# Kernel tuning notes

Hardware: AMD Instinct MI355X
Metric: run time of the kernel (lower is better)

Reference implementation:

```python
import jax, jax.numpy as jnp
import numpy as np

TOP_K = 8
H, E, I = 2048, 64, 768  # hidden, experts, moe_intermediate


def setup_inputs() -> dict:
    key = jax.random.key(0)
    k1, k2, k3, k4 = jax.random.split(key, 4)
    hidden_states = jax.random.normal(k1, (2, 256, H), dtype=jnp.float32)
    gate_w = jax.random.normal(k2, (E, H), dtype=jnp.float32) * 0.02   # nn.Linear(H, E).weight
    w13 = jax.random.normal(k3, (E, 2 * I, H), dtype=jnp.float32) * 0.02  # [E, 2I, H]
    w2 = jax.random.normal(k4, (E, H, I), dtype=jnp.float32) * 0.02       # [E, H, I]
    return {"hidden_states": hidden_states, "gate_w": gate_w, "w13": w13, "w2": w2}


def reference(hidden_states, gate_w, w13, w2):
    orig_shape = hidden_states.shape
    x = hidden_states.reshape(-1, orig_shape[-1])  # [M, H]
    M = x.shape[0]
    num_experts = gate_w.shape[0]

    # Router: logits -> fp32 softmax -> top-k -> renormalize
    router_logits = x @ gate_w.T  # [M, E]
    routing_weights = jax.nn.softmax(router_logits.astype(jnp.float32), axis=-1)
    topk_w, topk_ids = jax.lax.top_k(routing_weights, TOP_K)  # [M, K]
    topk_w = topk_w / jnp.sum(topk_w, axis=-1, keepdims=True)

    # Scatter top-k weights into a dense [M, E] combine matrix (zeros elsewhere),
    # equivalent to dispatch -> grouped expert FFN -> weighted combine.
    combine = jnp.zeros((M, num_experts), jnp.float32).at[
        jnp.arange(M)[:, None], topk_ids
    ].add(topk_w)

    # Expert FFN: gate/up projection, SiLU-gate, down projection.
    h = jnp.einsum('mh,eih->emi', x, w13)          # [E, M, 2I]
    g, u = jnp.split(h, 2, axis=-1)                # each [E, M, I]
    act = jax.nn.silu(g) * u                       # [E, M, I]
    expert_out = jnp.einsum('emi,ehi->emh', act, w2)  # [E, M, H]

    out = jnp.einsum('emh,me->mh', expert_out, combine)  # weighted combine
    return out.reshape(orig_shape)
```

## Files before the change

kernel.cpp:

```cpp
#include <hip/hip_runtime.h>
#include <hip/hip_bf16.h>

#define H_ 2048
#define E_ 64
#define I_ 768
#define K_ 8
#define GT 5
#define BKF 32

typedef __attribute__((ext_vector_type(8))) __bf16 bf16x8;
typedef __attribute__((ext_vector_type(4))) float f32x4;

__device__ inline unsigned short f2bfbits(float f) {
  unsigned u = __float_as_uint(f);
  u = (u + 0x7fffu + ((u >> 16) & 1u)) >> 16;
  return (unsigned short)u;
}
__device__ inline f32x4 mfma16(bf16x8 a, bf16x8 b, f32x4 c) {
  return __builtin_amdgcn_mfma_f32_16x16x32_bf16(a, b, c, 0, 0, 0);
}
__device__ inline bf16x8 packv(f32x4 a, f32x4 b) {
  union { unsigned u[4]; bf16x8 v; } r;
  asm("v_cvt_pk_bf16_f32 %0, %1, %2" : "=v"(r.u[0]) : "v"(a[0]), "v"(a[1]));
  asm("v_cvt_pk_bf16_f32 %0, %1, %2" : "=v"(r.u[1]) : "v"(a[2]), "v"(a[3]));
  asm("v_cvt_pk_bf16_f32 %0, %1, %2" : "=v"(r.u[2]) : "v"(b[0]), "v"(b[1]));
  asm("v_cvt_pk_bf16_f32 %0, %1, %2" : "=v"(r.u[3]) : "v"(b[2]), "v"(b[3]));
  return r.v;
}
__device__ inline void dma16(const float* g, float* l) {
  __builtin_amdgcn_global_load_lds(
      (const __attribute__((address_space(1))) float*)g,
      (__attribute__((address_space(3))) float*)l, 16, 0, 0);
}
#define SB() __builtin_amdgcn_sched_barrier(0)

__global__ __launch_bounds__(256) void router_kernel(
    const float* __restrict__ x, const float* __restrict__ gw,
    int* __restrict__ topk_id, float* __restrict__ topk_w,
    __hip_bfloat16* __restrict__ xb, int* __restrict__ cnt) {
  __shared__ float xs[H_];
  __shared__ float probs[E_];
  int m = blockIdx.x;
  if (m == 0 && threadIdx.x < E_) cnt[threadIdx.x] = 0;
  const float* xr = x + (size_t)m * H_;
  for (int i = threadIdx.x; i < H_; i += 256) xs[i] = xr[i];
  __syncthreads();
  unsigned short* xbr = reinterpret_cast<unsigned short*>(xb) + (size_t)m * H_;
  for (int i = threadIdx.x; i < H_; i += 256) xbr[i] = f2bfbits(xs[i]);
  int e = threadIdx.x >> 2, part = threadIdx.x & 3;
  const float* gr = gw + (size_t)e * H_ + part * (H_ / 4);
  const float* xx = xs + part * (H_ / 4);
  float s = 0.f;
#pragma unroll 8
  for (int i = 0; i < H_ / 4; ++i) s = fmaf(xx[i], gr[i], s);
  s += __shfl_xor(s, 1);
  s += __shfl_xor(s, 2);
  if (part == 0) probs[e] = s;
  __syncthreads();
  if (threadIdx.x == 0) {
    float mx = -1e30f;
    for (int i = 0; i < E_; ++i) mx = fmaxf(mx, probs[i]);
    float sum = 0.f;
    for (int i = 0; i < E_; ++i) { float p = expf(probs[i] - mx); probs[i] = p; sum += p; }
    float inv = 1.f / sum;
    for (int i = 0; i < E_; ++i) probs[i] *= inv;
    float bw[K_]; int bi[K_]; float wsum = 0.f;
#pragma unroll
    for (int k = 0; k < K_; ++k) {
      float best = -1.f; int b = 0;
      for (int i = 0; i < E_; ++i) if (probs[i] > best) { best = probs[i]; b = i; }
      bw[k] = best; bi[k] = b; wsum += best; probs[b] = -2.f;
    }
    float winv = 1.f / wsum;
#pragma unroll
    for (int k = 0; k < K_; ++k) {
      topk_id[m * K_ + k] = bi[k];
      topk_w[m * K_ + k] = bw[k] * winv;
    }
  }
}

__global__ void scatter_kernel(const int* __restrict__ topk_id, int* cnt,
                               int* perEx, int MK, int M) {
  int idx = blockIdx.x * 256 + threadIdx.x;
  if (idx >= MK) return;
  int e = topk_id[idx];
  int pos = atomicAdd(cnt + e, 1);
  perEx[e * M + pos] = idx;
}

__global__ void scan_kernel(const int* cnt, int* off) {
  if (threadIdx.x == 0) {
    int a = 0;
    for (int e = 0; e < E_; ++e) { off[e] = a; a += cnt[e]; }
    off[E_] = a;
  }
}

__global__ void compact_kernel(const int* __restrict__ cnt, const int* __restrict__ off,
                               const int* __restrict__ perEx,
                               int* __restrict__ entry_mk, int* __restrict__ slot2g, int M) {
  int e = blockIdx.x; int n = cnt[e]; int b = off[e];
  for (int p = threadIdx.x; p < n; p += 256) {
    int mk = perEx[e * M + p];
    entry_mk[b + p] = mk;
    slot2g[mk] = b + p;
  }
}

__global__ __launch_bounds__(256, 3) void gateup_mfma(
    const __hip_bfloat16* __restrict__ xb, const float* __restrict__ w13,
    const int* __restrict__ cnt, const int* __restrict__ off,
    const int* __restrict__ entry_mk, __hip_bfloat16* __restrict__ ACT) {
  __shared__ __align__(16) float lds[3 * 4 * 1024];
  int e = blockIdx.y;
  int ne = cnt[e];
  if (ne == 0) return;
  int base = off[e];
  int wv = threadIdx.x >> 6, lane = threadIdx.x & 63;
  int i0 = blockIdx.x * 64 + wv * 16;
  int col = lane & 15, kq = lane >> 4;
  const float* w13e = w13 + (size_t)e * (2 * I_) * H_;

  const float* dsrc[4];
#pragma unroll
  for (int q = 0; q < 4; ++q) {
    int r = (q & 1) * 8 + (lane >> 3);
    int j = (lane & 7) ^ ((lane >> 3) & 7);
    size_t row = (size_t)(i0 + r) + ((q >= 2) ? (size_t)I_ : (size_t)0);
    dsrc[q] = w13e + row * H_ + (size_t)(j * 4);
  }
  unsigned laneByte = (unsigned)((col * 8 + ((2 * kq) ^ (col & 7))) * 16);

  const int NCH = H_ / BKF;
  int ntile = (ne + 15) >> 4;
  for (int tb = 0; tb < ntile; tb += GT) {
    const __hip_bfloat16* arow0[GT];
#pragma unroll
    for (int t = 0; t < GT; ++t) {
      int p = (tb + t) * 16 + col;
      int pc = p < ne ? p : ne - 1;
      int tok = entry_mk[base + pc] >> 3;
      arow0[t] = xb + (size_t)tok * H_ + kq * 8;
    }
    f32x4 accg[GT], accu[GT];
#pragma unroll
    for (int t = 0; t < GT; ++t) {
      accg[t] = (f32x4){0.f, 0.f, 0.f, 0.f};
      accu[t] = (f32x4){0.f, 0.f, 0.f, 0.f};
    }
    bf16x8 aA[GT], aB[GT];
    int bc = 0;
#pragma unroll
    for (int q = 0; q < 4; ++q) dma16(dsrc[q], &lds[(0 * 4 + wv) * 1024 + q * 256]);
    SB();
#pragma unroll
    for (int t = 0; t < GT; ++t) aA[t] = *reinterpret_cast<const bf16x8*>(arow0[t]);
    SB();
#pragma unroll
    for (int q = 0; q < 4; ++q) dma16(dsrc[q] + BKF, &lds[(1 * 4 + wv) * 1024 + q * 256]);
    SB();

    auto stepG = [&](int n, bf16x8 (&ac)[GT], bf16x8 (&an)[GT], int mode) {
      if (mode <= 1) {
        size_t ka = (size_t)(n + 1) * BKF;
#pragma unroll
        for (int t = 0; t < GT; ++t)
          an[t] = *reinterpret_cast<const bf16x8*>(arow0[t] + ka);
        SB();
      }
      if (mode == 0) {
        int bn = (bc == 0) ? 2 : bc - 1;
        size_t ko = (size_t)(n + 2) * BKF;
#pragma unroll
        for (int q = 0; q < 4; ++q)
          dma16(dsrc[q] + ko, &lds[(bn * 4 + wv) * 1024 + q * 256]);
        SB();
      }
      if (mode == 0)      asm volatile("s_waitcnt vmcnt(13)" ::: "memory");
      else if (mode == 1) asm volatile("s_waitcnt vmcnt(9)" ::: "memory");
      else                asm volatile("s_waitcnt vmcnt(0)" ::: "memory");
      SB();
      unsigned a0 = (unsigned)(size_t)(&lds[(bc * 4 + wv) * 1024]) + laneByte;
      unsigned a1 = a0 ^ 16u;
      f32x4 g0, g1, u0, u1;
      asm volatile("ds_read_b128 %0, %1" : "=v"(g0) : "v"(a0));
      asm volatile("ds_read_b128 %0, %1" : "=v"(g1) : "v"(a1));
      asm volatile("ds_read_b128 %0, %1 offset:2048" : "=v"(u0) : "v"(a0));
      asm volatile("ds_read_b128 %0, %1 offset:2048" : "=v"(u1) : "v"(a1));
      asm volatile("s_waitcnt lgkmcnt(0)" ::: "memory");
      SB();
      bf16x8 bg = packv(g0, g1);
      bf16x8 bu = packv(u0, u1);
#pragma unroll
      for (int t = 0; t < GT; ++t) {
        accg[t] = mfma16(ac[t], bg, accg[t]);
        accu[t] = mfma16(ac[t], bu, accu[t]);
      }
      bc = (bc == 2) ? 0 : bc + 1;
    };

#pragma unroll 1
    for (int n = 0; n + 2 < NCH; n += 2) {
      stepG(n, aA, aB, 0);
      stepG(n + 1, aB, aA, 0);
    }
    stepG(NCH - 2, aA, aB, 1);
    stepG(NCH - 1, aB, aA, 2);

#pragma unroll
    for (int t = 0; t < GT; ++t) {
#pragma unroll
      for (int r = 0; r < 4; ++r) {
        int m = (tb + t) * 16 + kq * 4 + r;
        if (m < ne) {
          float gv = accg[t][r], uv = accu[t][r];
          float act = gv / (1.f + __expf(-gv)) * uv;
          reinterpret_cast<unsigned short*>(ACT)[(size_t)(base + m) * I_ + i0 + col] =
              f2bfbits(act);
        }
      }
    }
  }
}

__global__ __launch_bounds__(256, 3) void down_mfma(
    const __hip_bfloat16* __restrict__ ACT, const float* __restrict__ w2,
    const int* __restrict__ cnt, const int* __restrict__ off,
    float* __restrict__ OUTS) {
  __shared__ __align__(16) float lds[3 * 4 * 512];
  int e = blockIdx.y;
  int ne = cnt[e];
  if (ne == 0) return;
  int base = off[e];
  int wv = threadIdx.x >> 6, lane = threadIdx.x & 63;
  int h0 = blockIdx.x * 64 + wv * 16;
  int col = lane & 15, kq = lane >> 4;
  const float* w2e = w2 + (size_t)e * H_ * I_;

  const float* dsrc[2];
#pragma unroll
  for (int q = 0; q < 2; ++q) {
    int r = q * 8 + (lane >> 3);
    int j = (lane & 7) ^ ((lane >> 3) & 7);
    dsrc[q] = w2e + (size_t)(h0 + r) * I_ + (size_t)(j * 4);
  }
  unsigned laneByte = (unsigned)((col * 8 + ((2 * kq) ^ (col & 7))) * 16);

  const int NCH = I_ / BKF;
  int ntile = (ne + 15) >> 4;
  for (int tb = 0; tb < ntile; tb += GT) {
    const __hip_bfloat16* arow0[GT];
#pragma unroll
    for (int t = 0; t < GT; ++t) {
      int p = (tb + t) * 16 + col;
      int pc = p < ne ? p : ne - 1;
      arow0[t] = ACT + (size_t)(base + pc) * I_ + kq * 8;
    }
    f32x4 acc[GT];
#pragma unroll
    for (int t = 0; t < GT; ++t) acc[t] = (f32x4){0.f, 0.f, 0.f, 0.f};
    bf16x8 aA[GT], aB[GT];
    int bc = 0;
#pragma unroll
    for (int q = 0; q < 2; ++q) dma16(dsrc[q], &lds[(0 * 4 + wv) * 512 + q * 256]);
    SB();
#pragma unroll
    for (int t = 0; t < GT; ++t) aA[t] = *reinterpret_cast<const bf16x8*>(arow0[t]);
    SB();
#pragma unroll
    for (int q = 0; q < 2; ++q) dma16(dsrc[q] + BKF, &lds[(1 * 4 + wv) * 512 + q * 256]);
    SB();

    auto stepD = [&](int n, bf16x8 (&ac)[GT], bf16x8 (&an)[GT], int mode) {
      if (mode <= 1) {
        size_t ka = (size_t)(n + 1) * BKF;
#pragma unroll
        for (int t = 0; t < GT; ++t)
          an[t] = *reinterpret_cast<const bf16x8*>(arow0[t] + ka);
        SB();
      }
      if (mode == 0) {
        int bn = (bc == 0) ? 2 : bc - 1;
        size_t ko = (size_t)(n + 2) * BKF;
#pragma unroll
        for (int q = 0; q < 2; ++q)
          dma16(dsrc[q] + ko, &lds[(bn * 4 + wv) * 512 + q * 256]);
        SB();
      }
      if (mode == 0)      asm volatile("s_waitcnt vmcnt(9)" ::: "memory");
      else if (mode == 1) asm volatile("s_waitcnt vmcnt(7)" ::: "memory");
      else                asm volatile("s_waitcnt vmcnt(0)" ::: "memory");
      SB();
      unsigned a0 = (unsigned)(size_t)(&lds[(bc * 4 + wv) * 512]) + laneByte;
      unsigned a1 = a0 ^ 16u;
      f32x4 w0, w1;
      asm volatile("ds_read_b128 %0, %1" : "=v"(w0) : "v"(a0));
      asm volatile("ds_read_b128 %0, %1" : "=v"(w1) : "v"(a1));
      asm volatile("s_waitcnt lgkmcnt(0)" ::: "memory");
      SB();
      bf16x8 bw = packv(w0, w1);
#pragma unroll
      for (int t = 0; t < GT; ++t) acc[t] = mfma16(ac[t], bw, acc[t]);
      bc = (bc == 2) ? 0 : bc + 1;
    };

#pragma unroll 1
    for (int n = 0; n + 2 < NCH; n += 2) {
      stepD(n, aA, aB, 0);
      stepD(n + 1, aB, aA, 0);
    }
    stepD(NCH - 2, aA, aB, 1);
    stepD(NCH - 1, aB, aA, 2);

#pragma unroll
    for (int t = 0; t < GT; ++t) {
#pragma unroll
      for (int r = 0; r < 4; ++r) {
        int m = (tb + t) * 16 + kq * 4 + r;
        if (m < ne) {
          OUTS[(size_t)(base + m) * H_ + h0 + col] = acc[t][r];
        }
      }
    }
  }
}

__global__ __launch_bounds__(256) void combine_kernel(
    const float* __restrict__ OUTS, const float* __restrict__ topk_w,
    const int* __restrict__ slot2g, float* __restrict__ out) {
  int m = blockIdx.x;
  float w[K_]; int g[K_];
#pragma unroll
  for (int k = 0; k < K_; ++k) { w[k] = topk_w[m * K_ + k]; g[k] = slot2g[m * K_ + k]; }
  for (int h = threadIdx.x; h < H_; h += 256) {
    float s = 0.f;
#pragma unroll
    for (int k = 0; k < K_; ++k) s = fmaf(w[k], OUTS[(size_t)g[k] * H_ + h], s);
    out[(size_t)m * H_ + h] = s;
  }
}

extern "C" void kernel_launch(void* const* d_in, const int* in_sizes, int n_in,
                              void* d_out, int out_size, void* d_ws, size_t ws_size,
                              hipStream_t stream) {
  const float* x   = (const float*)d_in[0];
  const float* gw  = (const float*)d_in[1];
  const float* w13 = (const float*)d_in[2];
  const float* w2  = (const float*)d_in[3];
  float* out = (float*)d_out;

  const int M = in_sizes[0] / H_;
  const int MK = M * K_;

  char* ws = (char*)d_ws;
  size_t o = 0;
  auto alloc = [&](size_t bytes) { size_t r = o; o = (o + bytes + 255) & ~(size_t)255; return r; };
  int*   topk_id  = (int*)(ws + alloc((size_t)MK * 4));
  float* topk_w   = (float*)(ws + alloc((size_t)MK * 4));
  int*   cnt      = (int*)(ws + alloc(E_ * 4));
  int*   off      = (int*)(ws + alloc((E_ + 1) * 4));
  int*   perEx    = (int*)(ws + alloc((size_t)E_ * M * 4));
  int*   entry_mk = (int*)(ws + alloc((size_t)MK * 4));
  int*   slot2g   = (int*)(ws + alloc((size_t)MK * 4));
  __hip_bfloat16* xb  = (__hip_bfloat16*)(ws + alloc((size_t)M * H_ * 2));
  __hip_bfloat16* ACT = (__hip_bfloat16*)(ws + alloc((size_t)MK * I_ * 2));
  float* OUTS     = (float*)(ws + alloc((size_t)MK * H_ * 4));
  (void)ws_size; (void)n_in; (void)out_size;

  router_kernel<<<M, 256, 0, stream>>>(x, gw, topk_id, topk_w, xb, cnt);
  scatter_kernel<<<(MK + 255) / 256, 256, 0, stream>>>(topk_id, cnt, perEx, MK, M);
  scan_kernel<<<1, 64, 0, stream>>>(cnt, off);
  compact_kernel<<<E_, 256, 0, stream>>>(cnt, off, perEx, entry_mk, slot2g, M);
  gateup_mfma<<<dim3(I_ / 64, E_), 256, 0, stream>>>(xb, w13, cnt, off, entry_mk, ACT);
  down_mfma<<<dim3(H_ / 64, E_), 256, 0, stream>>>(ACT, w2, cnt, off, OUTS);
  combine_kernel<<<M, 256, 0, stream>>>(OUTS, topk_w, slot2g, out);
}
```

Before: 455.4 us.

## Restructure expert GEMMs with large block-shared double-buffered LDS stages

Replaces the per-wave triple-buffered 32-wide K chunks in the gate/up and down MFMA kernels with block-cooperative, double-buffered 128-wide K stages. Each stage is loaded by all waves into a large shared LDS buffer and synchronised with workgroup barriers. K stages are rotated by a per-block start offset to spread DRAM/channel traffic, and the gate/up token tile count grows from 5 to 6. The aim is fewer, larger DMA batches and deeper latency hiding. In exchange, occupancy drops to 1 block/CU for gate/up and 2 for down, and two barriers are added per stage.

```diff
diff --git a/kernel.cpp b/kernel.cpp
--- a/kernel.cpp
+++ b/kernel.cpp
@@ -5,8 +5,8 @@
 #define E_ 64
 #define I_ 768
 #define K_ 8
-#define GT 5
-#define BKF 32
+#define GT 6
+#define GTD 5
 
 typedef __attribute__((ext_vector_type(8))) __bf16 bf16x8;
 typedef __attribute__((ext_vector_type(4))) float f32x4;
@@ -32,7 +32,14 @@
       (const __attribute__((address_space(1))) float*)g,
       (__attribute__((address_space(3))) float*)l, 16, 0, 0);
 }
+template <int OFS>
+__device__ inline f32x4 dsr(unsigned addr) {
+  f32x4 d;
+  asm volatile("ds_read_b128 %0, %1 offset:%2" : "=v"(d) : "v"(addr), "n"(OFS));
+  return d;
+}
 #define SB() __builtin_amdgcn_sched_barrier(0)
+#define LGKM0() do { asm volatile("s_waitcnt lgkmcnt(0)" ::: "memory"); SB(); } while (0)
 
 __global__ __launch_bounds__(256) void router_kernel(
     const float* __restrict__ x, const float* __restrict__ gw,
@@ -108,38 +115,49 @@
   }
 }
 
-__global__ __launch_bounds__(256, 3) void gateup_mfma(
+__global__ __launch_bounds__(256, 1) void gateup_mfma(
     const __hip_bfloat16* __restrict__ xb, const float* __restrict__ w13,
     const int* __restrict__ cnt, const int* __restrict__ off,
     const int* __restrict__ entry_mk, __hip_bfloat16* __restrict__ ACT) {
-  __shared__ __align__(16) float lds[3 * 4 * 1024];
+  __shared__ __align__(16) float lds[2][16384];
+  const int NST = 16;
   int e = blockIdx.y;
   int ne = cnt[e];
   if (ne == 0) return;
   int base = off[e];
   int wv = threadIdx.x >> 6, lane = threadIdx.x & 63;
-  int i0 = blockIdx.x * 64 + wv * 16;
+  int i0 = blockIdx.x * 64;
   int col = lane & 15, kq = lane >> 4;
+  int half = lane >> 5, p = lane & 31;
   const float* w13e = w13 + (size_t)e * (2 * I_) * H_;
-
-  const float* dsrc[4];
-#pragma unroll
-  for (int q = 0; q < 4; ++q) {
-    int r = (q & 1) * 8 + (lane >> 3);
-    int j = (lane & 7) ^ ((lane >> 3) & 7);
-    size_t row = (size_t)(i0 + r) + ((q >= 2) ? (size_t)I_ : (size_t)0);
-    dsrc[q] = w13e + row * H_ + (size_t)(j * 4);
-  }
-  unsigned laneByte = (unsigned)((col * 8 + ((2 * kq) ^ (col & 7))) * 16);
-
-  const int NCH = H_ / BKF;
+  int st0 = (blockIdx.x * 7 + blockIdx.y * 3) & (NST - 1);
+
+  int rowC = (wv < 2) ? (i0 + 32 * wv + half) : (I_ + i0 + 32 * wv - 64 + half);
+  const float* wbase = w13e + (size_t)rowC * H_;
+  int xo[4];
+#pragma unroll
+  for (int j = 0; j < 4; ++j) xo[j] = (p ^ ((j << 1) | half)) * 4;
+
+  auto issueD = [&](int s, int b) {
+    int cs = s + st0; if (cs >= NST) cs -= NST;
+    const float* bs = wbase + cs * 128;
+#pragma unroll
+    for (int q = 0; q < 16; ++q)
+      dma16(bs + (size_t)(2 * q) * H_ + xo[q & 3], &lds[b][(16 * wv + q) * 256]);
+  };
+
+  unsigned laneOfs = (unsigned)((8 * wv + (col >> 1)) * 1024 + (col & 1) * 512 +
+                                (((kq * 2) ^ (col & 7)) * 16));
+  unsigned ldsBase = (unsigned)(size_t)(&lds[0][0]);
+  int icol = i0 + 16 * wv + col;
+
   int ntile = (ne + 15) >> 4;
   for (int tb = 0; tb < ntile; tb += GT) {
     const __hip_bfloat16* arow0[GT];
 #pragma unroll
     for (int t = 0; t < GT; ++t) {
-      int p = (tb + t) * 16 + col;
-      int pc = p < ne ? p : ne - 1;
+      int pt = (tb + t) * 16 + col;
+      int pc = pt < ne ? pt : ne - 1;
       int tok = entry_mk[base + pc] >> 3;
       arow0[t] = xb + (size_t)tok * H_ + kq * 8;
     }
@@ -149,64 +167,54 @@
       accg[t] = (f32x4){0.f, 0.f, 0.f, 0.f};
       accu[t] = (f32x4){0.f, 0.f, 0.f, 0.f};
     }
-    bf16x8 aA[GT], aB[GT];
-    int bc = 0;
-#pragma unroll
-    for (int q = 0; q < 4; ++q) dma16(dsrc[q], &lds[(0 * 4 + wv) * 1024 + q * 256]);
+    bf16x8 aS0[GT], aS1[GT], aS2[GT], aS3[GT];
+    auto loadA = [&](bf16x8 (&dst)[GT], int kf) {
+#pragma unroll
+      for (int t = 0; t < GT; ++t)
+        dst[t] = *reinterpret_cast<const bf16x8*>(arow0[t] + kf);
+    };
+    issueD(0, 0); SB();
+    { int k0 = st0 * 128;
+      loadA(aS0, k0); loadA(aS1, k0 + 32); loadA(aS2, k0 + 64); loadA(aS3, k0 + 96); }
     SB();
-#pragma unroll
-    for (int t = 0; t < GT; ++t) aA[t] = *reinterpret_cast<const bf16x8*>(arow0[t]);
-    SB();
-#pragma unroll
-    for (int q = 0; q < 4; ++q) dma16(dsrc[q] + BKF, &lds[(1 * 4 + wv) * 1024 + q * 256]);
-    SB();
-
-    auto stepG = [&](int n, bf16x8 (&ac)[GT], bf16x8 (&an)[GT], int mode) {
-      if (mode <= 1) {
-        size_t ka = (size_t)(n + 1) * BKF;
-#pragma unroll
-        for (int t = 0; t < GT; ++t)
-          an[t] = *reinterpret_cast<const bf16x8*>(arow0[t] + ka);
-        SB();
+    issueD(1, 1); SB();
+
+#define GJ(JOFS, AC)                                                     \
+    {                                                                    \
+      f32x4 g0 = dsr<(JOFS)>(a0), g1 = dsr<(JOFS)>(a1);                  \
+      f32x4 u0 = dsr<(JOFS) + 32768>(a0), u1 = dsr<(JOFS) + 32768>(a1);  \
+      LGKM0();                                                           \
+      bf16x8 bg = packv(g0, g1), bu = packv(u0, u1);                     \
+      _Pragma("unroll")                                                  \
+      for (int t = 0; t < GT; ++t) {                                     \
+        accg[t] = mfma16(AC[t], bg, accg[t]);                            \
+        accu[t] = mfma16(AC[t], bu, accu[t]);                            \
+      }                                                                  \
+    }
+
+    for (int s = 0; s < NST; ++s) {
+      if (s < NST - 1) { asm volatile("s_waitcnt vmcnt(34)" ::: "memory"); }
+      else             { asm volatile("s_waitcnt vmcnt(18)" ::: "memory"); }
+      SB();
+      __builtin_amdgcn_s_barrier();
+      SB();
+      unsigned a0 = ldsBase + (unsigned)((s & 1) * 65536) + laneOfs;
+      unsigned a1 = a0 ^ 16u;
+      GJ(0, aS0)
+      GJ(128, aS1)
+      GJ(256, aS2)
+      GJ(384, aS3)
+      if (s < NST - 1) {
+        int cn = s + 1 + st0; if (cn >= NST) cn -= NST;
+        int kn = cn * 128;
+        loadA(aS0, kn); loadA(aS1, kn + 32); loadA(aS2, kn + 64); loadA(aS3, kn + 96);
       }
-      if (mode == 0) {
-        int bn = (bc == 0) ? 2 : bc - 1;
-        size_t ko = (size_t)(n + 2) * BKF;
-#pragma unroll
-        for (int q = 0; q < 4; ++q)
-          dma16(dsrc[q] + ko, &lds[(bn * 4 + wv) * 1024 + q * 256]);
-        SB();
-      }
-      if (mode == 0)      asm volatile("s_waitcnt vmcnt(13)" ::: "memory");
-      else if (mode == 1) asm volatile("s_waitcnt vmcnt(9)" ::: "memory");
-      else                asm volatile("s_waitcnt vmcnt(0)" ::: "memory");
-      SB();
-      unsigned a0 = (unsigned)(size_t)(&lds[(bc * 4 + wv) * 1024]) + laneByte;
-      unsigned a1 = a0 ^ 16u;
-      f32x4 g0, g1, u0, u1;
-      asm volatile("ds_read_b128 %0, %1" : "=v"(g0) : "v"(a0));
-      asm volatile("ds_read_b128 %0, %1" : "=v"(g1) : "v"(a1));
-      asm volatile("ds_read_b128 %0, %1 offset:2048" : "=v"(u0) : "v"(a0));
-      asm volatile("ds_read_b128 %0, %1 offset:2048" : "=v"(u1) : "v"(a1));
-      asm volatile("s_waitcnt lgkmcnt(0)" ::: "memory");
-      SB();
-      bf16x8 bg = packv(g0, g1);
-      bf16x8 bu = packv(u0, u1);
-#pragma unroll
-      for (int t = 0; t < GT; ++t) {
-        accg[t] = mfma16(ac[t], bg, accg[t]);
-        accu[t] = mfma16(ac[t], bu, accu[t]);
-      }
-      bc = (bc == 2) ? 0 : bc + 1;
-    };
-
-#pragma unroll 1
-    for (int n = 0; n + 2 < NCH; n += 2) {
-      stepG(n, aA, aB, 0);
-      stepG(n + 1, aB, aA, 0);
-    }
-    stepG(NCH - 2, aA, aB, 1);
-    stepG(NCH - 1, aB, aA, 2);
+      SB();
+      __builtin_amdgcn_s_barrier();
+      SB();
+      if (s + 2 < NST) { issueD(s + 2, s & 1); SB(); }
+    }
+#undef GJ
 
 #pragma unroll
     for (int t = 0; t < GT; ++t) {
@@ -216,7 +224,7 @@
         if (m < ne) {
           float gv = accg[t][r], uv = accu[t][r];
           float act = gv / (1.f + __expf(-gv)) * uv;
-          reinterpret_cast<unsigned short*>(ACT)[(size_t)(base + m) * I_ + i0 + col] =
+          reinterpret_cast<unsigned short*>(ACT)[(size_t)(base + m) * I_ + icol] =
               f2bfbits(act);
         }
       }
@@ -224,102 +232,105 @@
   }
 }
 
-__global__ __launch_bounds__(256, 3) void down_mfma(
+__global__ __launch_bounds__(256, 2) void down_mfma(
     const __hip_bfloat16* __restrict__ ACT, const float* __restrict__ w2,
     const int* __restrict__ cnt, const int* __restrict__ off,
     float* __restrict__ OUTS) {
-  __shared__ __align__(16) float lds[3 * 4 * 512];
+  __shared__ __align__(16) float lds[2][8192];
+  const int NST = 6;
   int e = blockIdx.y;
   int ne = cnt[e];
   if (ne == 0) return;
   int base = off[e];
   int wv = threadIdx.x >> 6, lane = threadIdx.x & 63;
-  int h0 = blockIdx.x * 64 + wv * 16;
+  int h0 = blockIdx.x * 64;
   int col = lane & 15, kq = lane >> 4;
+  int half = lane >> 5, p = lane & 31;
   const float* w2e = w2 + (size_t)e * H_ * I_;
-
-  const float* dsrc[2];
-#pragma unroll
-  for (int q = 0; q < 2; ++q) {
-    int r = q * 8 + (lane >> 3);
-    int j = (lane & 7) ^ ((lane >> 3) & 7);
-    dsrc[q] = w2e + (size_t)(h0 + r) * I_ + (size_t)(j * 4);
-  }
-  unsigned laneByte = (unsigned)((col * 8 + ((2 * kq) ^ (col & 7))) * 16);
-
-  const int NCH = I_ / BKF;
+  int st0 = (int)((unsigned)(blockIdx.x + blockIdx.y * 5) % (unsigned)NST);
+
+  const float* wbase = w2e + (size_t)(h0 + 16 * wv + half) * I_;
+  int xo[4];
+#pragma unroll
+  for (int j = 0; j < 4; ++j) xo[j] = (p ^ ((j << 1) | half)) * 4;
+
+  auto issueD = [&](int s, int b) {
+    int cs = s + st0; if (cs >= NST) cs -= NST;
+    const float* bs = wbase + cs * 128;
+#pragma unroll
+    for (int q = 0; q < 8; ++q)
+      dma16(bs + (size_t)(2 * q) * I_ + xo[q & 3], &lds[b][(8 * wv + q) * 256]);
+  };
+
+  unsigned laneOfs = (unsigned)((8 * wv + (col >> 1)) * 1024 + (col & 1) * 512 +
+                                (((kq * 2) ^ (col & 7)) * 16));
+  unsigned ldsBase = (unsigned)(size_t)(&lds[0][0]);
+  int hcol = h0 + 16 * wv + col;
+
   int ntile = (ne + 15) >> 4;
-  for (int tb = 0; tb < ntile; tb += GT) {
-    const __hip_bfloat16* arow0[GT];
-#pragma unroll
-    for (int t = 0; t < GT; ++t) {
-      int p = (tb + t) * 16 + col;
-      int pc = p < ne ? p : ne - 1;
+  for (int tb = 0; tb < ntile; tb += GTD) {
+    const __hip_bfloat16* arow0[GTD];
+#pragma unroll
+    for (int t = 0; t < GTD; ++t) {
+      int pt = (tb + t) * 16 + col;
+      int pc = pt < ne ? pt : ne - 1;
       arow0[t] = ACT + (size_t)(base + pc) * I_ + kq * 8;
     }
-    f32x4 acc[GT];
-#pragma unroll
-    for (int t = 0; t < GT; ++t) acc[t] = (f32x4){0.f, 0.f, 0.f, 0.f};
-    bf16x8 aA[GT], aB[GT];
-    int bc = 0;
-#pragma unroll
-    for (int q = 0; q < 2; ++q) dma16(dsrc[q], &lds[(0 * 4 + wv) * 512 + q * 256]);
+    f32x4 acc[GTD];
+#pragma unroll
+    for (int t = 0; t < GTD; ++t) acc[t] = (f32x4){0.f, 0.f, 0.f, 0.f};
+    bf16x8 aS0[GTD], aS1[GTD], aS2[GTD], aS3[GTD];
+    auto loadA = [&](bf16x8 (&dst)[GTD], int kf) {
+#pragma unroll
+      for (int t = 0; t < GTD; ++t)
+        dst[t] = *reinterpret_cast<const bf16x8*>(arow0[t] + kf);
+    };
+    issueD(0, 0); SB();
+    { int k0 = st0 * 128;
+      loadA(aS0, k0); loadA(aS1, k0 + 32); loadA(aS2, k0 + 64); loadA(aS3, k0 + 96); }
     SB();
-#pragma unroll
-    for (int t = 0; t < GT; ++t) aA[t] = *reinterpret_cast<const bf16x8*>(arow0[t]);
-    SB();
-#pragma unroll
-    for (int q = 0; q < 2; ++q) dma16(dsrc[q] + BKF, &lds[(1 * 4 + wv) * 512 + q * 256]);
-    SB();
-
-    auto stepD = [&](int n, bf16x8 (&ac)[GT], bf16x8 (&an)[GT], int mode) {
-      if (mode <= 1) {
-        size_t ka = (size_t)(n + 1) * BKF;
-#pragma unroll
-        for (int t = 0; t < GT; ++t)
-          an[t] = *reinterpret_cast<const bf16x8*>(arow0[t] + ka);
-        SB();
+    issueD(1, 1); SB();
+
+#define DJ(JOFS, AC)                                                     \
+    {                                                                    \
+      f32x4 w0 = dsr<(JOFS)>(a0), w1 = dsr<(JOFS)>(a1);                  \
+      LGKM0();                                                           \
+      bf16x8 bw = packv(w0, w1);                                         \
+      _Pragma("unroll")                                                  \
+      for (int t = 0; t < GTD; ++t) acc[t] = mfma16(AC[t], bw, acc[t]);  \
+    }
+
+    for (int s = 0; s < NST; ++s) {
+      if (s < NST - 1) { asm volatile("s_waitcnt vmcnt(23)" ::: "memory"); }
+      else             { asm volatile("s_waitcnt vmcnt(15)" ::: "memory"); }
+      SB();
+      __builtin_amdgcn_s_barrier();
+      SB();
+      unsigned a0 = ldsBase + (unsigned)((s & 1) * 32768) + laneOfs;
+      unsigned a1 = a0 ^ 16u;
+      DJ(0, aS0)
+      DJ(128, aS1)
+      DJ(256, aS2)
+      DJ(384, aS3)
+      if (s < NST - 1) {
+        int cn = s + 1 + st0; if (cn >= NST) cn -= NST;
+        int kn = cn * 128;
+        loadA(aS0, kn); loadA(aS1, kn + 32); loadA(aS2, kn + 64); loadA(aS3, kn + 96);
       }
-      if (mode == 0) {
-        int bn = (bc == 0) ? 2 : bc - 1;
-        size_t ko = (size_t)(n + 2) * BKF;
-#pragma unroll
-        for (int q = 0; q < 2; ++q)
-          dma16(dsrc[q] + ko, &lds[(bn * 4 + wv) * 512 + q * 256]);
-        SB();
-      }
-      if (mode == 0)      asm volatile("s_waitcnt vmcnt(9)" ::: "memory");
-      else if (mode == 1) asm volatile("s_waitcnt vmcnt(7)" ::: "memory");
-      else                asm volatile("s_waitcnt vmcnt(0)" ::: "memory");
-      SB();
-      unsigned a0 = (unsigned)(size_t)(&lds[(bc * 4 + wv) * 512]) + laneByte;
-      unsigned a1 = a0 ^ 16u;
-      f32x4 w0, w1;
-      asm volatile("ds_read_b128 %0, %1" : "=v"(w0) : "v"(a0));
-      asm volatile("ds_read_b128 %0, %1" : "=v"(w1) : "v"(a1));
-      asm volatile("s_waitcnt lgkmcnt(0)" ::: "memory");
-      SB();
-      bf16x8 bw = packv(w0, w1);
-#pragma unroll
-      for (int t = 0; t < GT; ++t) acc[t] = mfma16(ac[t], bw, acc[t]);
-      bc = (bc == 2) ? 0 : bc + 1;
-    };
-
-#pragma unroll 1
-    for (int n = 0; n + 2 < NCH; n += 2) {
-      stepD(n, aA, aB, 0);
-      stepD(n + 1, aB, aA, 0);
-    }
-    stepD(NCH - 2, aA, aB, 1);
-    stepD(NCH - 1, aB, aA, 2);
-
-#pragma unroll
-    for (int t = 0; t < GT; ++t) {
+      SB();
+      __builtin_amdgcn_s_barrier();
+      SB();
+      if (s + 2 < NST) { issueD(s + 2, s & 1); SB(); }
+    }
+#undef DJ
+
+#pragma unroll
+    for (int t = 0; t < GTD; ++t) {
 #pragma unroll
       for (int r = 0; r < 4; ++r) {
         int m = (tb + t) * 16 + kq * 4 + r;
         if (m < ne) {
-          OUTS[(size_t)(base + m) * H_ + h0 + col] = acc[t][r];
+          OUTS[(size_t)(base + m) * H_ + hcol] = acc[t][r];
         }
       }
     }
```

Measured after the change: 428.0 us, median of 2. 6.0% less time.
